# Kernel tuning notes

Hardware: AMD Instinct MI355X
Metric: run time of the kernel (lower is better)

The kernel has to match this reference:

```python
import jax, jax.numpy as jnp
import numpy as np

NEG_SLOPE = 0.2


def setup_inputs() -> dict:
    key = jax.random.key(0)
    k1, k2, k3, k4, k5 = jax.random.split(key, 5)
    N, E = 50000, 800000
    IN, H, O = 128, 4, 32
    x = jax.random.normal(k1, (N, IN), dtype=jnp.float32)
    edge_index = jax.random.randint(k2, (2, E), 0, N, dtype=jnp.int64)
    weight = jax.random.normal(k3, (IN, H, O), dtype=jnp.float32) * 0.05
    att_weight = jax.random.normal(k4, (H, 2 * O), dtype=jnp.float32) * 0.05
    bias = jax.random.normal(k5, (H * O,), dtype=jnp.float32) * 0.05
    return {"x": x, "edge_index": edge_index, "weight": weight,
            "att_weight": att_weight, "bias": bias}


def reference(x, edge_index, weight, att_weight, bias):
    # GAT forward, eval mode (dropout=0), concat=True.
    N = x.shape[0]
    H, O = weight.shape[1], weight.shape[2]
    # Linear transform: [N, H, O]
    h = jnp.einsum('ni,iho->nho', x, weight)
    src, dst = edge_index[0], edge_index[1]  # message src -> dst
    h_i = h[dst]   # target features per edge  [E, H, O]
    h_j = h[src]   # source features per edge  [E, H, O]
    # Attention logits: leaky_relu(att . [h_i || h_j])  -> [E, H]
    a_i, a_j = att_weight[:, :O], att_weight[:, O:]
    alpha = jnp.einsum('eho,ho->eh', h_i, a_i) + jnp.einsum('eho,ho->eh', h_j, a_j)
    alpha = jax.nn.leaky_relu(alpha, NEG_SLOPE)
    # Segment softmax over incoming edges of each dst node.
    amax = jax.ops.segment_max(alpha, dst, num_segments=N)      # [N, H]
    ex = jnp.exp(alpha - amax[dst])                             # [E, H]
    denom = jax.ops.segment_sum(ex, dst, num_segments=N)        # [N, H]
    coef = ex / (denom[dst] + 1e-16)                            # [E, H]
    # Weighted scatter-aggregate of source messages.
    out = jax.ops.segment_sum(h_j * coef[..., None], dst, num_segments=N)  # [N, H, O]
    out = out.reshape(N, H * O) + bias
    return out
```

## Files before the change

kernel.cpp:

```cpp
#include <hip/hip_runtime.h>
#include <hip/hip_fp16.h>
#include <math.h>

#define NEG_SLOPE 0.2f

typedef __attribute__((ext_vector_type(8))) short bf16x8;
typedef __attribute__((ext_vector_type(4))) short short4v;
typedef __attribute__((ext_vector_type(4))) float f32x4;
typedef __attribute__((ext_vector_type(8))) unsigned short u16x8;

__device__ __forceinline__ float lrelu(float x) { return x > 0.f ? x : NEG_SLOPE * x; }

__device__ __forceinline__ short f2bf(float f) {
    unsigned u = __float_as_uint(f);
    u += 0x7fff + ((u >> 16) & 1);
    return (short)(u >> 16);
}

__global__ __launch_bounds__(256) void k_gemm(const float* __restrict__ x,
                                              const float* __restrict__ w,
                                              const float* __restrict__ att,
                                              __half* __restrict__ hout,
                                              float* __restrict__ adi,
                                              float* __restrict__ adj,
                                              int* __restrict__ gcur, int N) {
    __shared__ short SH[24576];
    const int t = threadIdx.x;
    const int row0 = blockIdx.x * 64;

    if (blockIdx.x == 0) gcur[t] = 0;

    #pragma unroll
    for (int i = 0; i < 8; ++i) {
        int idx = t + 256 * i;
        int r = idx >> 5, c4 = (idx & 31) * 4;
        float4 v = make_float4(0.f, 0.f, 0.f, 0.f);
        if (row0 + r < N) v = *(const float4*)(x + (size_t)(row0 + r) * 128 + c4);
        short4v sv;
        sv.x = f2bf(v.x); sv.y = f2bf(v.y); sv.z = f2bf(v.z); sv.w = f2bf(v.w);
        *(short4v*)&SH[(r * 128 + c4) ^ ((r & 7) << 3)] = sv;
    }
    {
        int c = t & 127, kh = (t >> 7) * 64;
        for (int kb = 0; kb < 16; ++kb) {
            int k = kh + kb * 4;
            short4v sv;
            sv.x = f2bf(w[(size_t)(k + 0) * 128 + c]);
            sv.y = f2bf(w[(size_t)(k + 1) * 128 + c]);
            sv.z = f2bf(w[(size_t)(k + 2) * 128 + c]);
            sv.w = f2bf(w[(size_t)(k + 3) * 128 + c]);
            *(short4v*)&SH[8192 + ((c * 128 + k) ^ ((c & 7) << 3))] = sv;
        }
    }
    __syncthreads();

    const int wv = t >> 6, lane = t & 63;
    const int lr = lane & 15, kg = lane >> 4;

    f32x4 acc[8];
    #pragma unroll
    for (int n = 0; n < 8; ++n) acc[n] = (f32x4){0.f, 0.f, 0.f, 0.f};

    #pragma unroll
    for (int kk = 0; kk < 4; ++kk) {
        const int k0 = kk * 32 + kg * 8;
        int r = wv * 16 + lr;
        bf16x8 a = *(const bf16x8*)&SH[(r * 128 + k0) ^ ((r & 7) << 3)];
        bf16x8 b[8];
        #pragma unroll
        for (int n = 0; n < 8; ++n) {
            int c = n * 16 + lr;
            b[n] = *(const bf16x8*)&SH[8192 + ((c * 128 + k0) ^ ((c & 7) << 3))];
        }
        #pragma unroll
        for (int n = 0; n < 8; ++n)
            acc[n] = __builtin_amdgcn_mfma_f32_16x16x32_bf16(a, b[n], acc[n], 0, 0, 0);
    }

    #pragma unroll
    for (int reg = 0; reg < 4; ++reg) {
        int r = row0 + wv * 16 + kg * 4 + reg;
        if (r < N) {
            __half* hp = hout + (size_t)r * 128 + lr;
            #pragma unroll
            for (int n = 0; n < 8; ++n)
                hp[n * 16] = __float2half(acc[n][reg]);
        }
    }

    __syncthreads();
    float* attF = (float*)&SH[8192];
    attF[t] = att[t];
    #pragma unroll
    for (int reg = 0; reg < 4; ++reg) {
        int row = wv * 16 + kg * 4 + reg;
        #pragma unroll
        for (int n = 0; n < 8; ++n) {
            int col = n * 16 + lr;
            SH[(row * 128 + col) ^ ((row & 7) << 3)] =
                (short)__half_as_ushort(__float2half(acc[n][reg]));
        }
    }
    __syncthreads();
    {
        int row = t >> 2, head = t & 3;
        int grow = row0 + row;
        if (grow < N) {
            float si = 0.f, sj = 0.f;
            #pragma unroll
            for (int j = 0; j < 32; ++j) {
                int jj = (j + row) & 31;
                float hv = __half2float(__ushort_as_half(
                    (unsigned short)SH[(row * 128 + head * 32 + jj) ^ ((row & 7) << 3)]));
                si += hv * attF[head * 64 + jj];
                sj += hv * attF[head * 64 + 32 + jj];
            }
            adi[grow * 4 + head] = si;
            adj[grow * 4 + head] = sj;
        }
    }
}

__global__ __launch_bounds__(512) void k_bin(const int* __restrict__ ei,
                                             int* __restrict__ gcur,
                                             unsigned* __restrict__ bins,
                                             int E, int nbkt, int cap) {
    __shared__ int lcnt[256];
    __shared__ int lbase[256];
    const int t = threadIdx.x;
    if (t < nbkt) lcnt[t] = 0;
    __syncthreads();

    const int e0 = blockIdx.x * 4096;
    const int ne = min(4096, E - e0);

    int bkt[8], rank[8];
    unsigned pk[8];
    #pragma unroll
    for (int k = 0; k < 8; ++k) {
        int idx = t + k * 512;
        if (idx < ne) {
            int e = e0 + idx;
            int src = ei[e], dst = ei[E + e];
            int b = dst >> 8;
            bkt[k] = b;
            pk[k] = ((unsigned)(dst & 255) << 24) | (unsigned)src;
            rank[k] = atomicAdd(&lcnt[b], 1);
        } else bkt[k] = -1;
    }
    __syncthreads();
    if (t < nbkt && lcnt[t] > 0) lbase[t] = atomicAdd(&gcur[t], lcnt[t]);
    __syncthreads();
    #pragma unroll
    for (int k = 0; k < 8; ++k) {
        if (bkt[k] >= 0)
            bins[(size_t)bkt[k] * cap + lbase[bkt[k]] + rank[k]] = pk[k];
    }
}

__global__ __launch_bounds__(512) void k_bucket(const unsigned* __restrict__ bins,
                                                const int* __restrict__ gcur,
                                                int* __restrict__ rowoff,
                                                int* __restrict__ csr_src,
                                                int N, int cap, int nbkt) {
    __shared__ int cnt[256];
    __shared__ int scn[256];
    __shared__ int cur[256];
    const int b = blockIdx.x, t = threadIdx.x;

    if (t < 256) scn[t] = (t < nbkt) ? gcur[t] : 0;
    __syncthreads();
    for (int off = 1; off < 256; off <<= 1) {
        int u = (t < 256 && t >= off) ? scn[t - off] : 0;
        __syncthreads();
        if (t < 256) scn[t] += u;
        __syncthreads();
    }
    const int base = (b == 0) ? 0 : scn[b - 1];
    const int sz = gcur[b];
    const unsigned* myb = bins + (size_t)b * cap;

    if (t < 256) cnt[t] = 0;
    __syncthreads();
    for (int i = t; i < sz; i += 512) atomicAdd(&cnt[myb[i] >> 24], 1);
    __syncthreads();
    int v = (t < 256) ? cnt[t] : 0;
    if (t < 256) scn[t] = v;
    __syncthreads();
    for (int off = 1; off < 256; off <<= 1) {
        int u = (t < 256 && t >= off) ? scn[t - off] : 0;
        __syncthreads();
        if (t < 256) scn[t] += u;
        __syncthreads();
    }
    if (t < 256) {
        int excl = scn[t] - v;
        int node = b * 256 + t;
        if (node < N) rowoff[node] = base + excl;
        if (node == N - 1) rowoff[N] = base + excl + v;
        cur[t] = excl;
    }
    __syncthreads();
    for (int i = t; i < sz; i += 512) {
        unsigned p = myb[i];
        int pos = atomicAdd(&cur[p >> 24], 1);
        csr_src[base + pos] = (int)(p & 0xFFFFFFu);
    }
}

__global__ __launch_bounds__(256) void k_node(const int* __restrict__ rowoff,
                                              const int* __restrict__ csr_src,
                                              const __half* __restrict__ h,
                                              const float* __restrict__ adi,
                                              const float* __restrict__ adjf,
                                              const float* __restrict__ bias,
                                              float* __restrict__ out, int N) {
    int node = (blockIdx.x * blockDim.x + threadIdx.x) >> 6;
    if (node >= N) return;
    const int lane = threadIdx.x & 63;
    const int q = lane >> 4, s = lane & 15;
    const int head = s >> 2;

    const int beg = rowoff[node];
    const int deg = rowoff[node + 1] - beg;
    const float ai = adi[node * 4 + head];

    float acc[8] = {0.f, 0.f, 0.f, 0.f, 0.f, 0.f, 0.f, 0.f};
    float dsum = 0.f;

    for (int i = 0; i < deg; i += 16) {
        int idx[4];
        float aj[4];
        u16x8 hv[4];
        #pragma unroll
        for (int b = 0; b < 4; ++b) {
            int ee = i + 4 * b + q;
            idx[b] = csr_src[beg + (ee < deg ? ee : 0)];
        }
        #pragma unroll
        for (int b = 0; b < 4; ++b) {
            aj[b] = adjf[idx[b] * 4 + head];
            hv[b] = *(const u16x8*)(h + (size_t)idx[b] * 128 + s * 8);
        }
        #pragma unroll
        for (int b = 0; b < 4; ++b) {
            int ee = i + 4 * b + q;
            float ex = (ee < deg) ? __expf(lrelu(ai + aj[b])) : 0.f;
            dsum += ex;
            #pragma unroll
            for (int k = 0; k < 8; ++k)
                acc[k] += __half2float(__ushort_as_half(hv[b][k])) * ex;
        }
    }

    #pragma unroll
    for (int k = 0; k < 8; ++k) {
        acc[k] += __shfl_xor(acc[k], 16);
        acc[k] += __shfl_xor(acc[k], 32);
    }
    dsum += __shfl_xor(dsum, 16);
    dsum += __shfl_xor(dsum, 32);

    if (q == 0) {
        float inv = 1.f / (dsum + 1e-16f);
        const float4* b4 = (const float4*)(bias + s * 8);
        float4 bv0 = b4[0], bv1 = b4[1];
        float4 o0 = make_float4(acc[0] * inv + bv0.x, acc[1] * inv + bv0.y,
                                acc[2] * inv + bv0.z, acc[3] * inv + bv0.w);
        float4 o1 = make_float4(acc[4] * inv + bv1.x, acc[5] * inv + bv1.y,
                                acc[6] * inv + bv1.z, acc[7] * inv + bv1.w);
        float4* op = (float4*)(out + (size_t)node * 128 + s * 8);
        op[0] = o0;
        op[1] = o1;
    }
}

extern "C" void kernel_launch(void* const* d_in, const int* in_sizes, int n_in,
                              void* d_out, int out_size, void* d_ws, size_t ws_size,
                              hipStream_t stream) {
    const float* x    = (const float*)d_in[0];
    const int*   ei   = (const int*)d_in[1];
    const float* w    = (const float*)d_in[2];
    const float* att  = (const float*)d_in[3];
    const float* bias = (const float*)d_in[4];

    const int N = in_sizes[0] / 128;
    const int E = in_sizes[1] / 2;

    const int NBKT = (N + 255) >> 8;
    const int CAP  = 8192;

    float* out = (float*)d_out;
    char*  wsb = (char*)d_ws;

    __half* h   = (__half*)wsb;
    float*  adi = (float*)(wsb + (size_t)N * 128 * 2);
    float*  adj = adi + (size_t)N * 4;
    int* rowoff   = (int*)(adj + (size_t)N * 4);
    int* csr_src  = rowoff + (N + 1);
    int* gcur     = csr_src + E;
    unsigned* bins = (unsigned*)(gcur + 256);

    k_gemm<<<(N + 63) / 64, 256, 0, stream>>>(x, w, att, h, adi, adj, gcur, N);

    k_bin<<<(E + 4095) / 4096, 512, 0, stream>>>(ei, gcur, bins, E, NBKT, CAP);
    k_bucket<<<NBKT, 512, 0, stream>>>(bins, gcur, rowoff, csr_src, N, CAP, NBKT);

    {
        long long total = (long long)N * 64;
        int blocks = (int)((total + 255) / 256);
        k_node<<<blocks, 256, 0, stream>>>(rowoff, csr_src, (const __half*)h,
                                           adi, adj, bias, out, N);
    }
}
```

Measured before the change: 78.84 us.

## Fuse bucket CSR build into node aggregation with 128-node buckets in LDS

Bucket size drops from 256 to 128 destination nodes, so there are up to 512 buckets. The per-bucket counting sort and the per-node softmax aggregation are merged into one kernel. The CSR source list lives in shared memory instead of global memory, which removes the global rowoff/csr_src writes and reads and one kernel launch. In exchange there are fewer, larger blocks (391 blocks of 512 threads), so occupancy and load balance may suffer. Edges are silently truncated if a bucket holds more than 3072.

```diff
diff --git a/kernel.cpp b/kernel.cpp
--- a/kernel.cpp
+++ b/kernel.cpp
@@ -28,7 +28,7 @@
     const int t = threadIdx.x;
     const int row0 = blockIdx.x * 64;
 
-    if (blockIdx.x == 0) gcur[t] = 0;
+    if (blockIdx.x == 0) { gcur[t] = 0; gcur[t + 256] = 0; }
 
     #pragma unroll
     for (int i = 0; i < 8; ++i) {
@@ -125,10 +125,10 @@
                                              int* __restrict__ gcur,
                                              unsigned* __restrict__ bins,
                                              int E, int nbkt, int cap) {
-    __shared__ int lcnt[256];
-    __shared__ int lbase[256];
+    __shared__ int lcnt[512];
+    __shared__ int lbase[512];
     const int t = threadIdx.x;
-    if (t < nbkt) lcnt[t] = 0;
+    lcnt[t] = 0;
     __syncthreads();
 
     const int e0 = blockIdx.x * 4096;
@@ -142,9 +142,9 @@
         if (idx < ne) {
             int e = e0 + idx;
             int src = ei[e], dst = ei[E + e];
-            int b = dst >> 8;
+            int b = dst >> 7;
             bkt[k] = b;
-            pk[k] = ((unsigned)(dst & 255) << 24) | (unsigned)src;
+            pk[k] = ((unsigned)(dst & 127) << 24) | (unsigned)src;
             rank[k] = atomicAdd(&lcnt[b], 1);
         } else bkt[k] = -1;
     }
@@ -158,120 +158,104 @@
     }
 }
 
-__global__ __launch_bounds__(512) void k_bucket(const unsigned* __restrict__ bins,
-                                                const int* __restrict__ gcur,
-                                                int* __restrict__ rowoff,
-                                                int* __restrict__ csr_src,
-                                                int N, int cap, int nbkt) {
-    __shared__ int cnt[256];
-    __shared__ int scn[256];
-    __shared__ int cur[256];
+#define CSR_MAX 3072
+
+__global__ __launch_bounds__(512, 4) void k_bucket_node(
+        const unsigned* __restrict__ bins,
+        const int* __restrict__ gcur,
+        const __half* __restrict__ h,
+        const float* __restrict__ adi,
+        const float* __restrict__ adjf,
+        const float* __restrict__ bias,
+        float* __restrict__ out, int N, int cap) {
+    __shared__ int csrL[CSR_MAX];
+    __shared__ int cnt[128];
+    __shared__ int beg[128];
+    __shared__ int cur[128];
     const int b = blockIdx.x, t = threadIdx.x;
-
-    if (t < 256) scn[t] = (t < nbkt) ? gcur[t] : 0;
-    __syncthreads();
-    for (int off = 1; off < 256; off <<= 1) {
-        int u = (t < 256 && t >= off) ? scn[t - off] : 0;
+    const int sz = min(gcur[b], CSR_MAX);
+    const unsigned* myb = bins + (size_t)b * cap;
+
+    if (t < 128) cnt[t] = 0;
+    __syncthreads();
+    for (int i = t; i < sz; i += 512) atomicAdd(&cnt[myb[i] >> 24], 1);
+    __syncthreads();
+    if (t < 128) cur[t] = cnt[t];
+    __syncthreads();
+    for (int off = 1; off < 128; off <<= 1) {
+        int u = (t < 128 && t >= off) ? cur[t - off] : 0;
         __syncthreads();
-        if (t < 256) scn[t] += u;
+        if (t < 128) cur[t] += u;
         __syncthreads();
     }
-    const int base = (b == 0) ? 0 : scn[b - 1];
-    const int sz = gcur[b];
-    const unsigned* myb = bins + (size_t)b * cap;
-
-    if (t < 256) cnt[t] = 0;
-    __syncthreads();
-    for (int i = t; i < sz; i += 512) atomicAdd(&cnt[myb[i] >> 24], 1);
-    __syncthreads();
-    int v = (t < 256) ? cnt[t] : 0;
-    if (t < 256) scn[t] = v;
-    __syncthreads();
-    for (int off = 1; off < 256; off <<= 1) {
-        int u = (t < 256 && t >= off) ? scn[t - off] : 0;
-        __syncthreads();
-        if (t < 256) scn[t] += u;
-        __syncthreads();
-    }
-    if (t < 256) {
-        int excl = scn[t] - v;
-        int node = b * 256 + t;
-        if (node < N) rowoff[node] = base + excl;
-        if (node == N - 1) rowoff[N] = base + excl + v;
-        cur[t] = excl;
-    }
+    if (t < 128) { beg[t] = cur[t] - cnt[t]; cur[t] = cur[t] - cnt[t]; }
     __syncthreads();
     for (int i = t; i < sz; i += 512) {
         unsigned p = myb[i];
         int pos = atomicAdd(&cur[p >> 24], 1);
-        csr_src[base + pos] = (int)(p & 0xFFFFFFu);
-    }
-}
-
-__global__ __launch_bounds__(256) void k_node(const int* __restrict__ rowoff,
-                                              const int* __restrict__ csr_src,
-                                              const __half* __restrict__ h,
-                                              const float* __restrict__ adi,
-                                              const float* __restrict__ adjf,
-                                              const float* __restrict__ bias,
-                                              float* __restrict__ out, int N) {
-    int node = (blockIdx.x * blockDim.x + threadIdx.x) >> 6;
-    if (node >= N) return;
-    const int lane = threadIdx.x & 63;
+        csrL[pos] = (int)(p & 0xFFFFFFu);
+    }
+    __syncthreads();
+
+    const int wv = t >> 6, lane = t & 63;
     const int q = lane >> 4, s = lane & 15;
     const int head = s >> 2;
 
-    const int beg = rowoff[node];
-    const int deg = rowoff[node + 1] - beg;
-    const float ai = adi[node * 4 + head];
-
-    float acc[8] = {0.f, 0.f, 0.f, 0.f, 0.f, 0.f, 0.f, 0.f};
-    float dsum = 0.f;
-
-    for (int i = 0; i < deg; i += 16) {
-        int idx[4];
-        float aj[4];
-        u16x8 hv[4];
-        #pragma unroll
-        for (int b = 0; b < 4; ++b) {
-            int ee = i + 4 * b + q;
-            idx[b] = csr_src[beg + (ee < deg ? ee : 0)];
-        }
-        #pragma unroll
-        for (int b = 0; b < 4; ++b) {
-            aj[b] = adjf[idx[b] * 4 + head];
-            hv[b] = *(const u16x8*)(h + (size_t)idx[b] * 128 + s * 8);
-        }
-        #pragma unroll
-        for (int b = 0; b < 4; ++b) {
-            int ee = i + 4 * b + q;
-            float ex = (ee < deg) ? __expf(lrelu(ai + aj[b])) : 0.f;
-            dsum += ex;
-            #pragma unroll
-            for (int k = 0; k < 8; ++k)
-                acc[k] += __half2float(__ushort_as_half(hv[b][k])) * ex;
-        }
-    }
-
-    #pragma unroll
-    for (int k = 0; k < 8; ++k) {
-        acc[k] += __shfl_xor(acc[k], 16);
-        acc[k] += __shfl_xor(acc[k], 32);
-    }
-    dsum += __shfl_xor(dsum, 16);
-    dsum += __shfl_xor(dsum, 32);
-
-    if (q == 0) {
-        float inv = 1.f / (dsum + 1e-16f);
-        const float4* b4 = (const float4*)(bias + s * 8);
-        float4 bv0 = b4[0], bv1 = b4[1];
-        float4 o0 = make_float4(acc[0] * inv + bv0.x, acc[1] * inv + bv0.y,
-                                acc[2] * inv + bv0.z, acc[3] * inv + bv0.w);
-        float4 o1 = make_float4(acc[4] * inv + bv1.x, acc[5] * inv + bv1.y,
-                                acc[6] * inv + bv1.z, acc[7] * inv + bv1.w);
-        float4* op = (float4*)(out + (size_t)node * 128 + s * 8);
-        op[0] = o0;
-        op[1] = o1;
+    for (int n = wv; n < 128; n += 8) {
+        int node = b * 128 + n;
+        if (node >= N) break;
+        const int bg = beg[n];
+        const int deg = cnt[n];
+        const float ai = adi[node * 4 + head];
+
+        float acc[8] = {0.f, 0.f, 0.f, 0.f, 0.f, 0.f, 0.f, 0.f};
+        float dsum = 0.f;
+
+        for (int i = 0; i < deg; i += 16) {
+            int idx[4];
+            float aj[4];
+            u16x8 hv[4];
+            #pragma unroll
+            for (int bb = 0; bb < 4; ++bb) {
+                int ee = i + 4 * bb + q;
+                idx[bb] = csrL[bg + (ee < deg ? ee : 0)];
+            }
+            #pragma unroll
+            for (int bb = 0; bb < 4; ++bb) {
+                aj[bb] = adjf[idx[bb] * 4 + head];
+                hv[bb] = *(const u16x8*)(h + (size_t)idx[bb] * 128 + s * 8);
+            }
+            #pragma unroll
+            for (int bb = 0; bb < 4; ++bb) {
+                int ee = i + 4 * bb + q;
+                float ex = (ee < deg) ? __expf(lrelu(ai + aj[bb])) : 0.f;
+                dsum += ex;
+                #pragma unroll
+                for (int k = 0; k < 8; ++k)
+                    acc[k] += __half2float(__ushort_as_half(hv[bb][k])) * ex;
+            }
+        }
+
+        #pragma unroll
+        for (int k = 0; k < 8; ++k) {
+            acc[k] += __shfl_xor(acc[k], 16);
+            acc[k] += __shfl_xor(acc[k], 32);
+        }
+        dsum += __shfl_xor(dsum, 16);
+        dsum += __shfl_xor(dsum, 32);
+
+        if (q == 0) {
+            float inv = 1.f / (dsum + 1e-16f);
+            const float4* b4 = (const float4*)(bias + s * 8);
+            float4 bv0 = b4[0], bv1 = b4[1];
+            float4 o0 = make_float4(acc[0] * inv + bv0.x, acc[1] * inv + bv0.y,
+                                    acc[2] * inv + bv0.z, acc[3] * inv + bv0.w);
+            float4 o1 = make_float4(acc[4] * inv + bv1.x, acc[5] * inv + bv1.y,
+                                    acc[6] * inv + bv1.z, acc[7] * inv + bv1.w);
+            float4* op = (float4*)(out + (size_t)node * 128 + s * 8);
+            op[0] = o0;
+            op[1] = o1;
+        }
     }
 }
 
@@ -287,8 +271,8 @@
     const int N = in_sizes[0] / 128;
     const int E = in_sizes[1] / 2;
 
-    const int NBKT = (N + 255) >> 8;
-    const int CAP  = 8192;
+    const int NBKT = (N + 127) >> 7;
+    const int CAP  = 4096;
 
     float* out = (float*)d_out;
     char*  wsb = (char*)d_ws;
@@ -296,20 +280,11 @@
     __half* h   = (__half*)wsb;
     float*  adi = (float*)(wsb + (size_t)N * 128 * 2);
     float*  adj = adi + (size_t)N * 4;
-    int* rowoff   = (int*)(adj + (size_t)N * 4);
-    int* csr_src  = rowoff + (N + 1);
-    int* gcur     = csr_src + E;
-    unsigned* bins = (unsigned*)(gcur + 256);
+    int* gcur   = (int*)(adj + (size_t)N * 4);
+    unsigned* bins = (unsigned*)(gcur + 512);
 
     k_gemm<<<(N + 63) / 64, 256, 0, stream>>>(x, w, att, h, adi, adj, gcur, N);
-
     k_bin<<<(E + 4095) / 4096, 512, 0, stream>>>(ei, gcur, bins, E, NBKT, CAP);
-    k_bucket<<<NBKT, 512, 0, stream>>>(bins, gcur, rowoff, csr_src, N, CAP, NBKT);
-
-    {
-        long long total = (long long)N * 64;
-        int blocks = (int)((total + 255) / 256);
-        k_node<<<blocks, 256, 0, stream>>>(rowoff, csr_src, (const __half*)h,
-                                           adi, adj, bias, out, N);
-    }
-}
+    k_bucket_node<<<NBKT, 512, 0, stream>>>(bins, gcur, (const __half*)h,
+                                            adi, adj, bias, out, N, CAP);
+}
```

New measurement: 78.93 us. About the same (+0.1%).
